# Optimization experiments

Measured on AMD Instinct MI355X. Metric: run time of the kernel, lower is better.

The kernel has to match this reference:

```python
import jax, jax.numpy as jnp
import numpy as np

B, S, E, H, C = 256, 512, 256, 512, 128

def setup_inputs() -> dict:
    key = jax.random.key(0)
    ks = jax.random.split(key, 8)
    s_ih = 1.0 / np.sqrt(E)
    s_hh = 1.0 / np.sqrt(H)
    s_o = 1.0 / np.sqrt(H)
    return {
        "batched_data": jax.random.normal(ks[0], (B, S, E), dtype=jnp.float32),
        "batched_label": jax.random.randint(ks[1], (B,), 0, C),
        "h0": jax.random.uniform(ks[2], (B, H), dtype=jnp.float32),  # torch.rand init state
        "W_ih": jax.random.uniform(ks[3], (3 * H, E), minval=-s_ih, maxval=s_ih),
        "W_hh": jax.random.uniform(ks[4], (3 * H, H), minval=-s_hh, maxval=s_hh),
        "b_ih": jax.random.uniform(ks[5], (3 * H,), minval=-s_ih, maxval=s_ih),
        "b_hh": jax.random.uniform(ks[6], (3 * H,), minval=-s_hh, maxval=s_hh),
        "W_out": jax.random.uniform(ks[7], (C, H), minval=-s_o, maxval=s_o),
        "b_out": jnp.zeros((C,), dtype=jnp.float32),
    }

def _gru_step(h, x_t, W_ih, W_hh, b_ih, b_hh):
    # standard GRUCell math (torch convention)
    gi = x_t @ W_ih.T + b_ih          # [B, 3H]
    gh = h @ W_hh.T + b_hh            # [B, 3H]
    i_r, i_z, i_n = jnp.split(gi, 3, axis=-1)
    h_r, h_z, h_n = jnp.split(gh, 3, axis=-1)
    r = jax.nn.sigmoid(i_r + h_r)
    z = jax.nn.sigmoid(i_z + h_z)
    n = jnp.tanh(i_n + r * h_n)
    return (1.0 - z) * n + z * h

def reference(batched_data, batched_label, h0, W_ih, W_hh, b_ih, b_hh, W_out, b_out):
    xs = jnp.transpose(batched_data, (1, 0, 2))  # [S, B, E] time-major

    def step(h, x_t):
        h_new = _gru_step(h, x_t, W_ih, W_hh, b_ih, b_hh)
        return h_new, None

    h_last, _ = jax.lax.scan(step, h0, xs)
    logits = h_last @ W_out.T + b_out  # only last-step logits matter (loop keeps only i == seqlen-1)

    # cross_entropy with ignore_index=0, reduction='mean' over non-ignored
    logp = jax.nn.log_softmax(logits, axis=-1)
    nll = -jnp.take_along_axis(logp, batched_label[:, None], axis=-1)[:, 0]
    mask = (batched_label != 0).astype(logits.dtype)
    loss = jnp.sum(nll * mask) / jnp.maximum(jnp.sum(mask), 1.0)

    ans = jnp.argmax(logits, axis=1)
    correct_percentage = jnp.sum(ans == batched_label).astype(jnp.float32) / batched_label.shape[0]
    return loss, correct_percentage
```

## Files before the change

kernel.cpp:

```cpp
#include <hip/hip_runtime.h>
#include <hip/hip_bf16.h>
#include <stdint.h>


typedef __attribute__((ext_vector_type(8))) short bf16x8;
typedef __attribute__((ext_vector_type(4))) float f32x4;

#define SWZ(r) (((r)&7) << 4)

static __device__ __forceinline__ unsigned short f2bf(float f) {
  unsigned x = __builtin_bit_cast(unsigned, f);
  return (unsigned short)((x + 0x7fffu + ((x >> 16) & 1u)) >> 16);
}
static __device__ __forceinline__ float bf2f(unsigned u) {
  return __builtin_bit_cast(float, u << 16);
}
static __device__ __forceinline__ void st_sys_u32(void* p, unsigned v) {
  asm volatile("global_store_dword %0, %1, off sc0 sc1" :: "v"(p), "v"(v) : "memory");
}
static __device__ __forceinline__ void ld_sys_u32(unsigned& d, const void* p) {
  asm volatile("global_load_dword %0, %1, off sc0 sc1" : "=v"(d) : "v"(p) : "memory");
}

__global__ __launch_bounds__(256, 1) void gru_persistent(
    const float* __restrict__ x, const float* __restrict__ h0,
    const float* __restrict__ Wih, const float* __restrict__ Whh,
    const float* __restrict__ bih, const float* __restrict__ bhh,
    unsigned* __restrict__ flags, unsigned short* __restrict__ hbuf) {
  __shared__ __align__(16) char ldsb[16 * 1536];
  __shared__ __align__(16) float cb[4 * 4 * 2 * 256];

  const int tid = threadIdx.x, wg = blockIdx.x;
  const int tm = wg & 15, cu = wg >> 4;
  const int wv = tid >> 6, ln = tid & 63;
  const int bm = tm << 4;
  const int d0 = cu << 5;

  unsigned* tfl = flags + tm * 32;
  const unsigned* fp = tfl + (ln & 15);
  char* hs0 = (char*)hbuf + (size_t)tm * 16384;
  char* hs1 = (char*)hbuf + 262144 + (size_t)tm * 16384;

  bf16x8 BF[3][2][6];
  {
    const int j = ln & 15, kg = ln >> 4;
#pragma unroll
    for (int g = 0; g < 3; ++g)
#pragma unroll
      for (int nf = 0; nf < 2; ++nf)
#pragma unroll
        for (int f = 0; f < 6; ++f) {
          const int R = g * 512 + d0 + nf * 16 + j;
          const float* src;
          if (f < 2) src = Wih + (size_t)R * 256 + (64 * wv + 32 * f + 8 * kg);
          else       src = Whh + (size_t)R * 512 + (128 * wv + 32 * (f - 2) + 8 * kg);
          bf16x8 v;
#pragma unroll
          for (int i = 0; i < 8; ++i) v[i] = (short)f2bf(src[i]);
          BF[g][nf][f] = v;
        }
  }

  const int dl = tid & 15, rr = tid >> 4;
  const int dd0 = d0 + dl, dd1 = d0 + 16 + dl;
  const float bR0 = bih[dd0] + bhh[dd0], bR1 = bih[dd1] + bhh[dd1];
  const float bZ0 = bih[512 + dd0] + bhh[512 + dd0], bZ1 = bih[512 + dd1] + bhh[512 + dd1];
  const float bNx0 = bih[1024 + dd0], bNx1 = bih[1024 + dd1];
  const float bNh0 = bhh[1024 + dd0], bNh1 = bhh[1024 + dd1];

  float hr0 = h0[(size_t)(bm + rr) * 512 + dd0];
  float hr1 = h0[(size_t)(bm + rr) * 512 + dd1];

  {
    unsigned a0 = f2bf(hr0), a1 = f2bf(hr1);
    unsigned p0 = __shfl_xor(a0, 1, 64), p1 = __shfl_xor(a1, 1, 64);
    if (!(dl & 1)) {
      st_sys_u32(hs0 + rr * 1024 + ((2 * dd0) ^ SWZ(rr)), a0 | (p0 << 16));
      st_sys_u32(hs0 + rr * 1024 + ((2 * dd1) ^ SWZ(rr)), a1 | (p1 << 16));
    }
  }
  const int xr = tid >> 4, xi = tid & 15;
  f32x4 xv[4];
  {
    const float* xb = x + ((size_t)(bm + xr) * 512 + 0) * 256 + xi * 16;
#pragma unroll
    for (int q = 0; q < 4; ++q) xv[q] = *(const f32x4*)(xb + 4 * q);
  }
  {
    char* rowb = ldsb + xr * 1536;
    bf16x8 xa, xc;
#pragma unroll
    for (int q = 0; q < 4; ++q) {
      xa[q] = (short)f2bf(xv[0][q]); xa[4 + q] = (short)f2bf(xv[1][q]);
      xc[q] = (short)f2bf(xv[2][q]); xc[4 + q] = (short)f2bf(xv[3][q]);
    }
    *(bf16x8*)(rowb + ((32 * xi) ^ SWZ(xr))) = xa;
    *(bf16x8*)(rowb + ((32 * xi + 16) ^ SWZ(xr))) = xc;
  }
  asm volatile("s_waitcnt vmcnt(0)" ::: "memory");
  __syncthreads();
  if (tid == 192) st_sys_u32(tfl + cu, 1u);
  unsigned fv = 0;
  if (wv == 3) ld_sys_u32(fv, fp);

  const int arow = ln & 15, kg = ln >> 4;

  for (int t = 0; t < 512; ++t) {
    const unsigned tgt = (unsigned)(t + 1);
    f32x4 aR[2] = {}, aZ[2] = {}, aNx[2] = {}, aNh[2] = {};

#define XPART()                                                                     \
  _Pragma("unroll")                                                                 \
  for (int fx = 0; fx < 2; ++fx) {                                                  \
    const int p = 128 * wv + 64 * fx + 16 * kg;                                     \
    bf16x8 a = *(const bf16x8*)(ldsb + arow * 1536 + (p ^ SWZ(arow)));              \
    _Pragma("unroll")                                                               \
    for (int nf = 0; nf < 2; ++nf) {                                                \
      aR[nf] = __builtin_amdgcn_mfma_f32_16x16x32_bf16(a, BF[0][nf][fx], aR[nf], 0, 0, 0); \
      aZ[nf] = __builtin_amdgcn_mfma_f32_16x16x32_bf16(a, BF[1][nf][fx], aZ[nf], 0, 0, 0); \
      aNx[nf] = __builtin_amdgcn_mfma_f32_16x16x32_bf16(a, BF[2][nf][fx], aNx[nf], 0, 0, 0); \
    }                                                                               \
  }

    if (wv == 3) {
      asm volatile("s_waitcnt vmcnt(0)" : "+v"(fv) :: "memory");
      while (__ballot(fv >= tgt) != ~0ull) {
        asm volatile("global_load_dword %0, %1, off sc0 sc1\n\ts_waitcnt vmcnt(0)"
                     : "=v"(fv) : "v"(fp) : "memory");
      }
    } else {
      XPART();
    }
    __syncthreads();

    const char* hsrc = (t & 1) ? hs1 : hs0;
    f32x4 t0, t1, t2, t3;
    asm volatile("global_load_dwordx4 %0, %1, off sc0 sc1"
                 : "=v"(t0) : "v"(hsrc + (wv * 4 + 0) * 1024 + ln * 16) : "memory");
    asm volatile("global_load_dwordx4 %0, %1, off sc0 sc1"
                 : "=v"(t1) : "v"(hsrc + (wv * 4 + 1) * 1024 + ln * 16) : "memory");
    asm volatile("global_load_dwordx4 %0, %1, off sc0 sc1"
                 : "=v"(t2) : "v"(hsrc + (wv * 4 + 2) * 1024 + ln * 16) : "memory");
    asm volatile("global_load_dwordx4 %0, %1, off sc0 sc1"
                 : "=v"(t3) : "v"(hsrc + (wv * 4 + 3) * 1024 + ln * 16) : "memory");

    if (wv == 3) { XPART(); }
    __builtin_amdgcn_sched_barrier(0);

    asm volatile("s_waitcnt vmcnt(0)" : "+v"(t0), "+v"(t1), "+v"(t2), "+v"(t3) :: "memory");
    *(f32x4*)(ldsb + (wv * 4 + 0) * 1536 + 512 + ln * 16) = t0;
    *(f32x4*)(ldsb + (wv * 4 + 1) * 1536 + 512 + ln * 16) = t1;
    *(f32x4*)(ldsb + (wv * 4 + 2) * 1536 + 512 + ln * 16) = t2;
    *(f32x4*)(ldsb + (wv * 4 + 3) * 1536 + 512 + ln * 16) = t3;
    __syncthreads();

    if (t + 1 < 512) {
      const float* xb2 = x + ((size_t)(bm + xr) * 512 + (t + 1)) * 256 + xi * 16;
#pragma unroll
      for (int q = 0; q < 4; ++q) xv[q] = *(const f32x4*)(xb2 + 4 * q);
    }

#pragma unroll
    for (int fh = 0; fh < 4; ++fh) {
      const int p = 512 + 256 * wv + 64 * fh + 16 * kg;
      bf16x8 a = *(const bf16x8*)(ldsb + arow * 1536 + (p ^ SWZ(arow)));
#pragma unroll
      for (int nf = 0; nf < 2; ++nf) {
        aR[nf] = __builtin_amdgcn_mfma_f32_16x16x32_bf16(a, BF[0][nf][2 + fh], aR[nf], 0, 0, 0);
        aZ[nf] = __builtin_amdgcn_mfma_f32_16x16x32_bf16(a, BF[1][nf][2 + fh], aZ[nf], 0, 0, 0);
        aNh[nf] = __builtin_amdgcn_mfma_f32_16x16x32_bf16(a, BF[2][nf][2 + fh], aNh[nf], 0, 0, 0);
      }
    }

    {
      const int cc = ln & 15, cg = ln >> 4;
#pragma unroll
      for (int nf = 0; nf < 2; ++nf)
#pragma unroll
        for (int i = 0; i < 4; ++i) {
          const int row = cg * 4 + i;
          cb[((wv * 4 + 0) * 2 + nf) * 256 + row * 16 + cc] = aR[nf][i];
          cb[((wv * 4 + 1) * 2 + nf) * 256 + row * 16 + cc] = aZ[nf][i];
          cb[((wv * 4 + 2) * 2 + nf) * 256 + row * 16 + cc] = aNx[nf][i];
          cb[((wv * 4 + 3) * 2 + nf) * 256 + row * 16 + cc] = aNh[nf][i];
        }
    }
    __syncthreads();

    {
#define CBX(w, ty, nf) cb[(((w) * 4 + (ty)) * 2 + (nf)) * 256 + rr * 16 + dl]
      float rp0 = bR0 + CBX(0,0,0) + CBX(1,0,0) + CBX(2,0,0) + CBX(3,0,0);
      float rp1 = bR1 + CBX(0,0,1) + CBX(1,0,1) + CBX(2,0,1) + CBX(3,0,1);
      float zp0 = bZ0 + CBX(0,1,0) + CBX(1,1,0) + CBX(2,1,0) + CBX(3,1,0);
      float zp1 = bZ1 + CBX(0,1,1) + CBX(1,1,1) + CBX(2,1,1) + CBX(3,1,1);
      float ix0 = bNx0 + CBX(0,2,0) + CBX(1,2,0) + CBX(2,2,0) + CBX(3,2,0);
      float ix1 = bNx1 + CBX(0,2,1) + CBX(1,2,1) + CBX(2,2,1) + CBX(3,2,1);
      float hn0 = bNh0 + CBX(0,3,0) + CBX(1,3,0) + CBX(2,3,0) + CBX(3,3,0);
      float hn1 = bNh1 + CBX(0,3,1) + CBX(1,3,1) + CBX(2,3,1) + CBX(3,3,1);
#undef CBX
      const float rg0 = 1.f / (1.f + __expf(-rp0)), rg1 = 1.f / (1.f + __expf(-rp1));
      const float zg0 = 1.f / (1.f + __expf(-zp0)), zg1 = 1.f / (1.f + __expf(-zp1));
      const float e0 = __expf(2.f * (ix0 + rg0 * hn0));
      const float e1 = __expf(2.f * (ix1 + rg1 * hn1));
      const float ng0 = 1.f - 2.f / (e0 + 1.f), ng1 = 1.f - 2.f / (e1 + 1.f);
      hr0 = ng0 + zg0 * (hr0 - ng0);
      hr1 = ng1 + zg1 * (hr1 - ng1);
    }

    {
      char* hdst = ((t + 1) & 1) ? hs1 : hs0;
      unsigned a0 = f2bf(hr0), a1 = f2bf(hr1);
      unsigned p0 = __shfl_xor(a0, 1, 64), p1 = __shfl_xor(a1, 1, 64);
      if (!(dl & 1)) {
        st_sys_u32(hdst + rr * 1024 + ((2 * dd0) ^ SWZ(rr)), a0 | (p0 << 16));
        st_sys_u32(hdst + rr * 1024 + ((2 * dd1) ^ SWZ(rr)), a1 | (p1 << 16));
      }
    }
    if (t + 1 < 512) {
      char* rowb = ldsb + xr * 1536;
      bf16x8 xa, xc;
#pragma unroll
      for (int q = 0; q < 4; ++q) {
        xa[q] = (short)f2bf(xv[0][q]); xa[4 + q] = (short)f2bf(xv[1][q]);
        xc[q] = (short)f2bf(xv[2][q]); xc[4 + q] = (short)f2bf(xv[3][q]);
      }
      *(bf16x8*)(rowb + ((32 * xi) ^ SWZ(xr))) = xa;
      *(bf16x8*)(rowb + ((32 * xi + 16) ^ SWZ(xr))) = xc;
    }
    asm volatile("s_waitcnt vmcnt(0)" ::: "memory");
    __syncthreads();
    if (tid == 192) st_sys_u32(tfl + cu, tgt + 1u);
    if (wv == 3) ld_sys_u32(fv, fp);
  }
#undef XPART
}

__global__ __launch_bounds__(128) void logits_loss(
    const unsigned short* __restrict__ hbuf, const float* __restrict__ Wout,
    const float* __restrict__ bout, const int* __restrict__ label,
    float* __restrict__ accv) {
  __shared__ float hrow[512];
  __shared__ float lg[128];
  const int b = blockIdx.x;
  const int tm = b >> 4, r = b & 15;
  const char* base = (const char*)hbuf + (size_t)tm * 16384 + r * 1024;
  for (int i = threadIdx.x; i < 256; i += 128) {
    const char* p = base + ((i * 4) ^ SWZ(r));
    unsigned v;
    asm volatile("global_load_dword %0, %1, off sc0 sc1\n\ts_waitcnt vmcnt(0)"
                 : "=v"(v) : "v"(p) : "memory");
    hrow[2 * i] = bf2f(v & 0xffffu);
    hrow[2 * i + 1] = bf2f(v >> 16);
  }
  __syncthreads();
  const int c = threadIdx.x;
  const f32x4* w4 = (const f32x4*)(Wout + (size_t)c * 512);
  const f32x4* h4 = (const f32x4*)hrow;
  float s = bout[c];
#pragma unroll 4
  for (int i = 0; i < 128; ++i) {
    f32x4 wv = w4[i], hv = h4[i];
    s += wv[0] * hv[0] + wv[1] * hv[1] + wv[2] * hv[2] + wv[3] * hv[3];
  }
  lg[c] = s;
  __syncthreads();
  if (c == 0) {
    float mx = lg[0];
    int am = 0;
    for (int i = 1; i < 128; ++i)
      if (lg[i] > mx) { mx = lg[i]; am = i; }
    float se = 0.f;
    for (int i = 0; i < 128; ++i) se += __expf(lg[i] - mx);
    const int lb = label[b];
    const float logp = lg[lb] - mx - __logf(se);
    if (lb != 0) {
      atomicAdd(&accv[0], -logp);
      atomicAdd(&accv[1], 1.0f);
    }
    if (am == lb) atomicAdd(&accv[2], 1.0f);
  }
}

__global__ void finalize_k(const float* __restrict__ accv, float* __restrict__ out) {
  out[0] = accv[0] / fmaxf(accv[1], 1.0f);
  out[1] = accv[2] * (1.0f / 256.0f);
}

extern "C" void kernel_launch(void* const* d_in, const int* in_sizes, int n_in,
                              void* d_out, int out_size, void* d_ws, size_t ws_size,
                              hipStream_t stream) {
  (void)in_sizes; (void)n_in; (void)out_size; (void)ws_size;
  const float* x = (const float*)d_in[0];
  const int* label = (const int*)d_in[1];
  const float* h0 = (const float*)d_in[2];
  const float* Wih = (const float*)d_in[3];
  const float* Whh = (const float*)d_in[4];
  const float* bih = (const float*)d_in[5];
  const float* bhh = (const float*)d_in[6];
  const float* Wout = (const float*)d_in[7];
  const float* bout = (const float*)d_in[8];
  float* out = (float*)d_out;

  char* ws = (char*)d_ws;
  unsigned* flags = (unsigned*)ws;
  float* accv = (float*)(ws + 4096);
  unsigned short* hbuf = (unsigned short*)(ws + 8192);

  hipMemsetAsync(ws, 0, 8192, stream);

  gru_persistent<<<dim3(256), dim3(256), 0, stream>>>(x, h0, Wih, Whh, bih, bhh,
                                                      flags, hbuf);
  logits_loss<<<dim3(256), dim3(128), 0, stream>>>(hbuf, Wout, bout, label, accv);
  finalize_k<<<dim3(1), dim3(1), 0, stream>>>(accv, out);
}
```

Baseline: 1.447 ms.

## Load MFMA A-fragments directly into registers, bypassing LDS staging

The hidden state is now loaded from global memory straight into the per-lane MFMA A-operand layout using swizzled offsets. The x input is also loaded per lane into register fragments, so the LDS staging buffer and one block-wide barrier per step go away. This shortens the serial per-timestep critical path of the recurrence. In exchange, global loads become per-lane 16-byte gathers across rows instead of contiguous row copies, and register pressure rises.

```diff
diff --git a/kernel.cpp b/kernel.cpp
--- a/kernel.cpp
+++ b/kernel.cpp
@@ -20,6 +20,15 @@
 }
 static __device__ __forceinline__ void ld_sys_u32(unsigned& d, const void* p) {
   asm volatile("global_load_dword %0, %1, off sc0 sc1" : "=v"(d) : "v"(p) : "memory");
+}
+static __device__ __forceinline__ bf16x8 cvt8(f32x4 a, f32x4 b) {
+  bf16x8 r;
+#pragma unroll
+  for (int q = 0; q < 4; ++q) {
+    r[q] = (short)f2bf(a[q]);
+    r[4 + q] = (short)f2bf(b[q]);
+  }
+  return r;
 }
 
 __global__ __launch_bounds__(256, 1) void gru_persistent(
@@ -27,7 +36,6 @@
     const float* __restrict__ Wih, const float* __restrict__ Whh,
     const float* __restrict__ bih, const float* __restrict__ bhh,
     unsigned* __restrict__ flags, unsigned short* __restrict__ hbuf) {
-  __shared__ __align__(16) char ldsb[16 * 1536];
   __shared__ __align__(16) float cb[4 * 4 * 2 * 256];
 
   const int tid = threadIdx.x, wg = blockIdx.x;
@@ -43,7 +51,7 @@
 
   bf16x8 BF[3][2][6];
   {
-    const int j = ln & 15, kg = ln >> 4;
+    const int j = ln & 15, kgw = ln >> 4;
 #pragma unroll
     for (int g = 0; g < 3; ++g)
 #pragma unroll
@@ -52,8 +60,8 @@
         for (int f = 0; f < 6; ++f) {
           const int R = g * 512 + d0 + nf * 16 + j;
           const float* src;
-          if (f < 2) src = Wih + (size_t)R * 256 + (64 * wv + 32 * f + 8 * kg);
-          else       src = Whh + (size_t)R * 512 + (128 * wv + 32 * (f - 2) + 8 * kg);
+          if (f < 2) src = Wih + (size_t)R * 256 + (64 * wv + 32 * f + 8 * kgw);
+          else       src = Whh + (size_t)R * 512 + (128 * wv + 32 * (f - 2) + 8 * kgw);
           bf16x8 v;
 #pragma unroll
           for (int i = 0; i < 8; ++i) v[i] = (short)f2bf(src[i]);
@@ -71,6 +79,13 @@
   float hr0 = h0[(size_t)(bm + rr) * 512 + dd0];
   float hr1 = h0[(size_t)(bm + rr) * 512 + dd1];
 
+  const int grow = ln & 15, kg = ln >> 4;
+  const int gof0 = grow * 1024 + ((256 * wv + 0 + 16 * kg) ^ SWZ(grow));
+  const int gof1 = grow * 1024 + ((256 * wv + 64 + 16 * kg) ^ SWZ(grow));
+  const int gof2 = grow * 1024 + ((256 * wv + 128 + 16 * kg) ^ SWZ(grow));
+  const int gof3 = grow * 1024 + ((256 * wv + 192 + 16 * kg) ^ SWZ(grow));
+  const float* xlane = x + (size_t)(bm + grow) * 512 * 256 + 64 * wv + 8 * kg;
+
   {
     unsigned a0 = f2bf(hr0), a1 = f2bf(hr1);
     unsigned p0 = __shfl_xor(a0, 1, 64), p1 = __shfl_xor(a1, 1, 64);
@@ -79,47 +94,34 @@
       st_sys_u32(hs0 + rr * 1024 + ((2 * dd1) ^ SWZ(rr)), a1 | (p1 << 16));
     }
   }
-  const int xr = tid >> 4, xi = tid & 15;
-  f32x4 xv[4];
-  {
-    const float* xb = x + ((size_t)(bm + xr) * 512 + 0) * 256 + xi * 16;
-#pragma unroll
-    for (int q = 0; q < 4; ++q) xv[q] = *(const f32x4*)(xb + 4 * q);
-  }
-  {
-    char* rowb = ldsb + xr * 1536;
-    bf16x8 xa, xc;
-#pragma unroll
-    for (int q = 0; q < 4; ++q) {
-      xa[q] = (short)f2bf(xv[0][q]); xa[4 + q] = (short)f2bf(xv[1][q]);
-      xc[q] = (short)f2bf(xv[2][q]); xc[4 + q] = (short)f2bf(xv[3][q]);
-    }
-    *(bf16x8*)(rowb + ((32 * xi) ^ SWZ(xr))) = xa;
-    *(bf16x8*)(rowb + ((32 * xi + 16) ^ SWZ(xr))) = xc;
-  }
+  f32x4 xn0a = *(const f32x4*)(xlane + 0);
+  f32x4 xn0b = *(const f32x4*)(xlane + 4);
+  f32x4 xn1a = *(const f32x4*)(xlane + 32);
+  f32x4 xn1b = *(const f32x4*)(xlane + 36);
+  bf16x8 xf0 = cvt8(xn0a, xn0b);
+  bf16x8 xf1 = cvt8(xn1a, xn1b);
+
   asm volatile("s_waitcnt vmcnt(0)" ::: "memory");
   __syncthreads();
   if (tid == 192) st_sys_u32(tfl + cu, 1u);
   unsigned fv = 0;
   if (wv == 3) ld_sys_u32(fv, fp);
 
-  const int arow = ln & 15, kg = ln >> 4;
-
   for (int t = 0; t < 512; ++t) {
     const unsigned tgt = (unsigned)(t + 1);
     f32x4 aR[2] = {}, aZ[2] = {}, aNx[2] = {}, aNh[2] = {};
 
-#define XPART()                                                                     \
-  _Pragma("unroll")                                                                 \
-  for (int fx = 0; fx < 2; ++fx) {                                                  \
-    const int p = 128 * wv + 64 * fx + 16 * kg;                                     \
-    bf16x8 a = *(const bf16x8*)(ldsb + arow * 1536 + (p ^ SWZ(arow)));              \
-    _Pragma("unroll")                                                               \
-    for (int nf = 0; nf < 2; ++nf) {                                                \
-      aR[nf] = __builtin_amdgcn_mfma_f32_16x16x32_bf16(a, BF[0][nf][fx], aR[nf], 0, 0, 0); \
-      aZ[nf] = __builtin_amdgcn_mfma_f32_16x16x32_bf16(a, BF[1][nf][fx], aZ[nf], 0, 0, 0); \
-      aNx[nf] = __builtin_amdgcn_mfma_f32_16x16x32_bf16(a, BF[2][nf][fx], aNx[nf], 0, 0, 0); \
-    }                                                                               \
+#define XPART()                                                                          \
+  {                                                                                      \
+    _Pragma("unroll")                                                                    \
+    for (int nf = 0; nf < 2; ++nf) {                                                     \
+      aR[nf]  = __builtin_amdgcn_mfma_f32_16x16x32_bf16(xf0, BF[0][nf][0], aR[nf], 0, 0, 0);  \
+      aZ[nf]  = __builtin_amdgcn_mfma_f32_16x16x32_bf16(xf0, BF[1][nf][0], aZ[nf], 0, 0, 0);  \
+      aNx[nf] = __builtin_amdgcn_mfma_f32_16x16x32_bf16(xf0, BF[2][nf][0], aNx[nf], 0, 0, 0); \
+      aR[nf]  = __builtin_amdgcn_mfma_f32_16x16x32_bf16(xf1, BF[0][nf][1], aR[nf], 0, 0, 0);  \
+      aZ[nf]  = __builtin_amdgcn_mfma_f32_16x16x32_bf16(xf1, BF[1][nf][1], aZ[nf], 0, 0, 0);  \
+      aNx[nf] = __builtin_amdgcn_mfma_f32_16x16x32_bf16(xf1, BF[2][nf][1], aNx[nf], 0, 0, 0); \
+    }                                                                                    \
   }
 
     if (wv == 3) {
@@ -134,42 +136,48 @@
     __syncthreads();
 
     const char* hsrc = (t & 1) ? hs1 : hs0;
-    f32x4 t0, t1, t2, t3;
+    f32x4 g0, g1, g2, g3;
     asm volatile("global_load_dwordx4 %0, %1, off sc0 sc1"
-                 : "=v"(t0) : "v"(hsrc + (wv * 4 + 0) * 1024 + ln * 16) : "memory");
+                 : "=v"(g0) : "v"(hsrc + gof0) : "memory");
     asm volatile("global_load_dwordx4 %0, %1, off sc0 sc1"
-                 : "=v"(t1) : "v"(hsrc + (wv * 4 + 1) * 1024 + ln * 16) : "memory");
+                 : "=v"(g1) : "v"(hsrc + gof1) : "memory");
     asm volatile("global_load_dwordx4 %0, %1, off sc0 sc1"
-                 : "=v"(t2) : "v"(hsrc + (wv * 4 + 2) * 1024 + ln * 16) : "memory");
+                 : "=v"(g2) : "v"(hsrc + gof2) : "memory");
     asm volatile("global_load_dwordx4 %0, %1, off sc0 sc1"
-                 : "=v"(t3) : "v"(hsrc + (wv * 4 + 3) * 1024 + ln * 16) : "memory");
+                 : "=v"(g3) : "v"(hsrc + gof3) : "memory");
 
     if (wv == 3) { XPART(); }
     __builtin_amdgcn_sched_barrier(0);
 
-    asm volatile("s_waitcnt vmcnt(0)" : "+v"(t0), "+v"(t1), "+v"(t2), "+v"(t3) :: "memory");
-    *(f32x4*)(ldsb + (wv * 4 + 0) * 1536 + 512 + ln * 16) = t0;
-    *(f32x4*)(ldsb + (wv * 4 + 1) * 1536 + 512 + ln * 16) = t1;
-    *(f32x4*)(ldsb + (wv * 4 + 2) * 1536 + 512 + ln * 16) = t2;
-    *(f32x4*)(ldsb + (wv * 4 + 3) * 1536 + 512 + ln * 16) = t3;
-    __syncthreads();
+    asm volatile("s_waitcnt vmcnt(0)"
+                 : "+v"(g0), "+v"(g1), "+v"(g2), "+v"(g3) :: "memory");
+    const bf16x8 hf0 = __builtin_bit_cast(bf16x8, g0);
+    const bf16x8 hf1 = __builtin_bit_cast(bf16x8, g1);
+    const bf16x8 hf2 = __builtin_bit_cast(bf16x8, g2);
+    const bf16x8 hf3 = __builtin_bit_cast(bf16x8, g3);
 
     if (t + 1 < 512) {
-      const float* xb2 = x + ((size_t)(bm + xr) * 512 + (t + 1)) * 256 + xi * 16;
-#pragma unroll
-      for (int q = 0; q < 4; ++q) xv[q] = *(const f32x4*)(xb2 + 4 * q);
-    }
-
-#pragma unroll
-    for (int fh = 0; fh < 4; ++fh) {
-      const int p = 512 + 256 * wv + 64 * fh + 16 * kg;
-      bf16x8 a = *(const bf16x8*)(ldsb + arow * 1536 + (p ^ SWZ(arow)));
-#pragma unroll
-      for (int nf = 0; nf < 2; ++nf) {
-        aR[nf] = __builtin_amdgcn_mfma_f32_16x16x32_bf16(a, BF[0][nf][2 + fh], aR[nf], 0, 0, 0);
-        aZ[nf] = __builtin_amdgcn_mfma_f32_16x16x32_bf16(a, BF[1][nf][2 + fh], aZ[nf], 0, 0, 0);
-        aNh[nf] = __builtin_amdgcn_mfma_f32_16x16x32_bf16(a, BF[2][nf][2 + fh], aNh[nf], 0, 0, 0);
-      }
+      const float* xb2 = xlane + (size_t)(t + 1) * 256;
+      xn0a = *(const f32x4*)(xb2 + 0);
+      xn0b = *(const f32x4*)(xb2 + 4);
+      xn1a = *(const f32x4*)(xb2 + 32);
+      xn1b = *(const f32x4*)(xb2 + 36);
+    }
+
+#pragma unroll
+    for (int nf = 0; nf < 2; ++nf) {
+      aR[nf]  = __builtin_amdgcn_mfma_f32_16x16x32_bf16(hf0, BF[0][nf][2], aR[nf], 0, 0, 0);
+      aZ[nf]  = __builtin_amdgcn_mfma_f32_16x16x32_bf16(hf0, BF[1][nf][2], aZ[nf], 0, 0, 0);
+      aNh[nf] = __builtin_amdgcn_mfma_f32_16x16x32_bf16(hf0, BF[2][nf][2], aNh[nf], 0, 0, 0);
+      aR[nf]  = __builtin_amdgcn_mfma_f32_16x16x32_bf16(hf1, BF[0][nf][3], aR[nf], 0, 0, 0);
+      aZ[nf]  = __builtin_amdgcn_mfma_f32_16x16x32_bf16(hf1, BF[1][nf][3], aZ[nf], 0, 0, 0);
+      aNh[nf] = __builtin_amdgcn_mfma_f32_16x16x32_bf16(hf1, BF[2][nf][3], aNh[nf], 0, 0, 0);
+      aR[nf]  = __builtin_amdgcn_mfma_f32_16x16x32_bf16(hf2, BF[0][nf][4], aR[nf], 0, 0, 0);
+      aZ[nf]  = __builtin_amdgcn_mfma_f32_16x16x32_bf16(hf2, BF[1][nf][4], aZ[nf], 0, 0, 0);
+      aNh[nf] = __builtin_amdgcn_mfma_f32_16x16x32_bf16(hf2, BF[2][nf][4], aNh[nf], 0, 0, 0);
+      aR[nf]  = __builtin_amdgcn_mfma_f32_16x16x32_bf16(hf3, BF[0][nf][5], aR[nf], 0, 0, 0);
+      aZ[nf]  = __builtin_amdgcn_mfma_f32_16x16x32_bf16(hf3, BF[1][nf][5], aZ[nf], 0, 0, 0);
+      aNh[nf] = __builtin_amdgcn_mfma_f32_16x16x32_bf16(hf3, BF[2][nf][5], aNh[nf], 0, 0, 0);
     }
 
     {
@@ -217,15 +225,8 @@
       }
     }
     if (t + 1 < 512) {
-      char* rowb = ldsb + xr * 1536;
-      bf16x8 xa, xc;
-#pragma unroll
-      for (int q = 0; q < 4; ++q) {
-        xa[q] = (short)f2bf(xv[0][q]); xa[4 + q] = (short)f2bf(xv[1][q]);
-        xc[q] = (short)f2bf(xv[2][q]); xc[4 + q] = (short)f2bf(xv[3][q]);
-      }
-      *(bf16x8*)(rowb + ((32 * xi) ^ SWZ(xr))) = xa;
-      *(bf16x8*)(rowb + ((32 * xi + 16) ^ SWZ(xr))) = xc;
+      xf0 = cvt8(xn0a, xn0b);
+      xf1 = cvt8(xn1a, xn1b);
     }
     asm volatile("s_waitcnt vmcnt(0)" ::: "memory");
     __syncthreads();
```

Measured after the change: 1.316 ms. -9.0%, faster.
